# Performance work log

Measured on AMD Instinct MI355X. Metric: run time of the kernel, lower is better.

## Reference

```python
import jax, jax.numpy as jnp
import numpy as np
from itertools import product

# Static geometry (matches init_kwargs)
Z, H, W = 8, 96, 180
WZ, WH, WW = 2, 6, 12
MZ, MH, MW = Z // WZ, H // WH, W // WW   # 4, 16, 15
WP = WZ * WH * WW                        # 144 tokens per window
WN = MZ * MH * MW                        # 960 windows
DIM, HEADS = 384, 12
DH = DIM // HEADS
SHIFT = (WZ // 2, WH // 2, WW // 2)      # (1, 3, 6)
NBIAS = WZ * WZ * WH * WH * (2 * WW - 1) # 3312 bias entries
WT = MZ * MH                             # 64 window types (vary with Z,H only)


def _position_index():
    zi = np.arange(WZ); zj = -np.arange(WZ) * WZ
    hi = np.arange(WH); hj = -np.arange(WH) * WH
    w = np.arange(WW)
    c1 = np.stack(np.meshgrid(zi, hi, w, indexing='ij')).reshape(3, WP, 1)
    c2 = np.stack(np.meshgrid(zj, hj, w, indexing='ij')).reshape(3, 1, WP)
    coords = (c1 - c2).transpose(1, 2, 0).astype(np.int64)  # (WP, WP, 3)
    coords[:, :, 2] += WW - 1
    coords[:, :, 1] *= 2 * WW - 1
    coords[:, :, 0] *= (2 * WW - 1) * WH * WH
    return coords.sum(-1).reshape(-1)  # (WP*WP,)


def _attention_mask():
    # in_shape divisible by window -> pad mask is all-zero; only shifted-window
    # (non-adjacency) mask remains, exactly as in the torch buffer.
    img = np.ones((Z, H, W), np.float32)
    zs = (slice(0, -WZ), slice(-WZ, -SHIFT[0]), slice(-SHIFT[0], None))
    hs = (slice(0, -WH), slice(-WH, -SHIFT[1]), slice(-SHIFT[1], None))
    ws = (slice(0, -WW), slice(-WW, -SHIFT[2]), slice(-SHIFT[2], None))
    cnt = 0
    for z, h, w in product(zs, hs, ws):
        img[z, h, w] = cnt
        cnt += 1
    mw = img.reshape(MZ, WZ, MH, WH, MW, WW).transpose(0, 2, 4, 1, 3, 5).reshape(WN, WP)
    diff = mw[:, None, :] - mw[:, :, None]
    return np.where(diff != 0, -100.0, 0.0).astype(np.float32)


POS_IDX = jnp.asarray(_position_index())
ATTN_MASK = jnp.asarray(_attention_mask())  # (WN, WP, WP)


def _layernorm(x, w, b, eps=1e-5):
    m = jnp.mean(x, axis=-1, keepdims=True)
    v = jnp.mean(jnp.square(x - m), axis=-1, keepdims=True)
    return (x - m) * jax.lax.rsqrt(v + eps) * w + b


def setup_inputs() -> dict:
    key = jax.random.key(0)
    ks = jax.random.split(key, 8)
    s = 0.02
    return {
        'x': jax.random.normal(ks[0], (1, Z * H * W, DIM), jnp.float32),
        'w_qkv': jax.random.normal(ks[1], (DIM, 3 * DIM), jnp.float32) * s,
        'w_proj': jax.random.normal(ks[2], (DIM, DIM), jnp.float32) * s,
        'b_proj': jnp.zeros((DIM,), jnp.float32),
        'bias_table': jax.random.normal(ks[3], (NBIAS, WT, HEADS), jnp.float32) * 0.02,
        'ln1_w': jnp.ones((DIM,), jnp.float32),
        'ln1_b': jnp.zeros((DIM,), jnp.float32),
        'ln2_w': jnp.ones((DIM,), jnp.float32),
        'ln2_b': jnp.zeros((DIM,), jnp.float32),
        'w1': jax.random.normal(ks[4], (DIM, 4 * DIM), jnp.float32) * s,
        'b1': jnp.zeros((4 * DIM,), jnp.float32),
        'w2': jax.random.normal(ks[5], (4 * DIM, DIM), jnp.float32) * s,
        'b2': jnp.zeros((DIM,), jnp.float32),
    }


def reference(x, w_qkv, w_proj, b_proj, bias_table, ln1_w, ln1_b, ln2_w, ln2_b, w1, b1, w2, b2):
    B = x.shape[0]
    shortcut = x
    # (B, Z*H*W, D) -> (B, Z, H, W, D); pad is identity (divisible shapes)
    xg = x.reshape(B, Z, H, W, DIM)
    xg = jnp.roll(xg, (-SHIFT[0], -SHIFT[1], -SHIFT[2]), axis=(1, 2, 3))
    # window partition -> (B*WN, WP, D) with window order (B, mZ, mH, mW)
    xw = xg.reshape(B, MZ, WZ, MH, WH, MW, WW, DIM)
    xw = xw.transpose(0, 1, 3, 5, 2, 4, 6, 7).reshape(B * WN, WP, DIM)

    # ---- EarthAttention3D ----
    qkv = (xw @ w_qkv).reshape(B * WN, WP, 3, HEADS, DH).transpose(2, 0, 3, 1, 4)
    q = qkv[0] * (DH ** -0.5)
    k, v = qkv[1], qkv[2]
    attn = jnp.einsum('bhid,bhjd->bhij', q, k)  # (B*WN, HEADS, WP, WP)

    # earth-specific bias: one bias per (mZ, mH) window type, shared over B, mW
    bias = bias_table[POS_IDX].reshape(WP, WP, WT, HEADS).transpose(2, 3, 0, 1)
    bias = bias.reshape(MZ, MH, HEADS, WP, WP)
    attn = attn.reshape(B, MZ, MH, MW, HEADS, WP, WP) + bias[None, :, :, None]

    # shifted-window mask
    attn = attn.reshape(B, WN, HEADS, WP, WP) + ATTN_MASK[None, :, None]
    attn = jax.nn.softmax(attn, axis=-1).reshape(B * WN, HEADS, WP, WP)

    out = jnp.einsum('bhij,bhjd->bhid', attn, v)
    out = out.transpose(0, 2, 1, 3).reshape(B * WN, WP, DIM)
    out = out @ w_proj + b_proj

    # ---- window reverse, unroll, crop (identity) ----
    xg = out.reshape(B, MZ, MH, MW, WZ, WH, WW, DIM)
    xg = xg.transpose(0, 1, 4, 2, 5, 3, 6, 7).reshape(B, Z, H, W, DIM)
    xg = jnp.roll(xg, SHIFT, axis=(1, 2, 3))
    attn_out = xg.reshape(B, Z * H * W, DIM)

    # Pangu post-norm residuals (drop_path prob = 0 -> identity)
    x = shortcut + _layernorm(attn_out, ln1_w, ln1_b)
    h = jax.nn.gelu(x @ w1 + b1, approximate=False) @ w2 + b2
    x = x + _layernorm(h, ln2_w, ln2_b)
    return x
```

## Files before the change

kernel.cpp:

```cpp
#include <hip/hip_runtime.h>
#include <hip/hip_bf16.h>
#include <math.h>

typedef __hip_bfloat16 bf16;
typedef __attribute__((ext_vector_type(4))) float f32x4;
typedef __attribute__((ext_vector_type(8))) short s16x8;
typedef __attribute__((ext_vector_type(4))) short s16x4;

#define DEVI __device__ __forceinline__

constexpr int ZD = 8, HD = 96, WD = 180;
constexpr int WZ = 2, WH = 6, WWn = 12;
constexpr int MZ = 4, MH = 16, MW = 15;
constexpr int WP = 144, WN = 960;
constexpr int DIM = 384, HEADS = 12, DH = 32;
constexpr int TOK = ZD * HD * WD;
constexpr size_t TOKDIM = (size_t)TOK * DIM;
constexpr int NC = 3, CM = TOK / NC;

DEVI short f2b(float f) {
    bf16 h = __float2bfloat16(f);
    return *reinterpret_cast<short*>(&h);
}

DEVI int row_to_token(int r) {
    int wn = r / WP;
    int p  = r - wn * WP;
    int mz = wn / (MH * MW);
    int rem = wn - mz * (MH * MW);
    int mh = rem / MW;
    int mw = rem - mh * MW;
    int lz = p / (WH * WWn);
    int rp = p - lz * (WH * WWn);
    int lh = rp / WWn;
    int lw = rp - lh * WWn;
    int zp = mz * WZ + lz + 1;  if (zp >= ZD) zp -= ZD;
    int hp = mh * WH + lh + 3;  if (hp >= HD) hp -= HD;
    int wp = mw * WWn + lw + 6; if (wp >= WD) wp -= WD;
    return (zp * HD + hp) * WD + wp;
}


__global__ __launch_bounds__(256)
void k_fill(float* __restrict__ out, int n, float v) {
    int i = blockIdx.x * blockDim.x + threadIdx.x;
    if (i < n) out[i] = v;
}

__global__ __launch_bounds__(256)
void k_wcast(const float* __restrict__ w, bf16* __restrict__ wt, int K, int N) {
    int idx = blockIdx.x * blockDim.x + threadIdx.x;
    if (idx >= K * N) return;
    int n = idx / K;
    int k = idx - n * K;
    wt[idx] = __float2bfloat16(w[(size_t)k * N + n]);
}

__global__ __launch_bounds__(256)
void k_btr(const float* __restrict__ bt, float* __restrict__ btr) {
    int idx = blockIdx.x * blockDim.x + threadIdx.x;
    if (idx >= 64 * 12 * 3312) return;
    int wth = idx / 3312;
    int pos = idx - wth * 3312;
    btr[idx] = bt[(size_t)pos * 768 + wth] * 1.4426950408889634f;
}

__global__ __launch_bounds__(256)
void k_mktab(const float* __restrict__ btr, bf16* __restrict__ tab) {
    int idx = blockIdx.x * blockDim.x + threadIdx.x;
    if (idx >= 768 * WP * WP) return;
    int t = idx / (WP * WP);
    int e = idx - t * (WP * WP);
    int i = e / WP, j = e - i * WP;
    int wt = t / 12;
    int mz = wt >> 4, mh = wt & 15;
    int lzi = i / 72, ri_ = i - lzi * 72, lhi = ri_ / 12, lwi = ri_ - lhi * 12;
    int lzj = j / 72, rj_ = j - lzj * 72, lhj = rj_ / 12, lwj = rj_ - lhj * 12;
    int cA = lzi * 828 + lhi * 23 + lwi;
    int cB = lzj * 1656 + lhj * 138 + (11 - lwj);
    float vv = btr[(size_t)t * 3312 + cA + cB];
    int zri = (mz == 3) ? (lzi + 1) : 0, zrj = (mz == 3) ? (lzj + 1) : 0;
    int hri = (mh == 15) ? (lhi < 3 ? 1 : 2) : 0, hrj = (mh == 15) ? (lhj < 3 ? 1 : 2) : 0;
    if (zri != zrj || hri != hrj) vv -= 144.26950408889634f;
    tab[idx] = __float2bfloat16(vv);
}

__global__ __launch_bounds__(256)
void k_gather_x(const float* __restrict__ x, bf16* __restrict__ xw) {
    int idx = blockIdx.x * blockDim.x + threadIdx.x;
    if (idx >= TOK * 96) return;
    int r  = idx / 96;
    int c4 = (idx - r * 96) * 4;
    int t  = row_to_token(r);
    const float4 vv = *(const float4*)(x + (size_t)t * DIM + c4);
    s16x4 o;
    o[0] = f2b(vv.x); o[1] = f2b(vv.y); o[2] = f2b(vv.z); o[3] = f2b(vv.w);
    *(s16x4*)((short*)xw + (size_t)r * DIM + c4) = o;
}


DEVI void gload16(const bf16* g, bf16* l) {
    __builtin_amdgcn_global_load_lds(
        (const __attribute__((address_space(1))) void*)g,
        (__attribute__((address_space(3))) void*)l, 16, 0, 0);
}

template <int EPI>
__global__ __launch_bounds__(256)
void k_gemm(const bf16* __restrict__ A, const bf16* __restrict__ BT,
            const float* __restrict__ bias, bf16* __restrict__ out,
            int M, int N, int K) {
    constexpr int BK = 64;
    __shared__ bf16 As[128 * BK];
    __shared__ bf16 Bs[128 * BK];

    const int nb = N >> 7;
    const int g = blockIdx.x;
    const int xcd = g & 7;
    const int ii = g >> 3;
    const int tt = ii / nb;
    const int bm = tt * 8 + xcd;
    const int bn = ii - tt * nb;

    const int tid = threadIdx.x;
    const int lane = tid & 63;
    const int wv = tid >> 6;
    const int wr = wv >> 1, wc = wv & 1;
    const int lg = lane >> 4, lc = lane & 15;

    const bf16* Ab = A + (size_t)bm * 128 * K;
    const bf16* Bb = BT + (size_t)bn * 128 * K;

    f32x4 acc[4][4];
#pragma unroll
    for (int mi = 0; mi < 4; mi++)
#pragma unroll
        for (int ni = 0; ni < 4; ni++) acc[mi][ni] = {0.f, 0.f, 0.f, 0.f};

    const int kiters = K / BK;
    const int srow = (lane >> 3);
    const int scol = (lane & 7) * 8;

    for (int kt = 0; kt < kiters; kt++) {
        const int k0 = kt * BK;
#pragma unroll
        for (int i = 0; i < 4; i++) {
            int ch = wv * 4 + i;
            int row = ch * 8 + srow;
            gload16(Ab + (size_t)row * K + k0 + scol, &As[ch * 512]);
            gload16(Bb + (size_t)row * K + k0 + scol, &Bs[ch * 512]);
        }
        asm volatile("s_waitcnt vmcnt(0)" ::: "memory");
        __syncthreads();
#pragma unroll
        for (int kk = 0; kk < 2; kk++) {
            s16x8 af[4], bfv[4];
#pragma unroll
            for (int mi = 0; mi < 4; mi++)
                af[mi] = *(const s16x8*)&As[(64 * wr + 16 * mi + lc) * BK + kk * 32 + 8 * lg];
#pragma unroll
            for (int ni = 0; ni < 4; ni++)
                bfv[ni] = *(const s16x8*)&Bs[(64 * wc + 16 * ni + lc) * BK + kk * 32 + 8 * lg];
#pragma unroll
            for (int mi = 0; mi < 4; mi++)
#pragma unroll
                for (int ni = 0; ni < 4; ni++)
                    acc[mi][ni] = __builtin_amdgcn_mfma_f32_16x16x32_bf16(
                        af[mi], bfv[ni], acc[mi][ni], 0, 0, 0);
        }
        __syncthreads();
    }

    const int rbase = bm * 128 + 64 * wr + 4 * lg;
    const int cbase = bn * 128 + 64 * wc + lc;
#pragma unroll
    for (int mi = 0; mi < 4; mi++) {
#pragma unroll
        for (int ni = 0; ni < 4; ni++) {
            const int gc = cbase + 16 * ni;
#pragma unroll
            for (int r2 = 0; r2 < 4; r2++) {
                const int gr = rbase + 16 * mi + r2;
                float val = acc[mi][ni][r2];
                if constexpr (EPI == 0) {
                    int which = gc / DIM;
                    int remc = gc - which * DIM;
                    int hh = remc >> 5, dh = remc & 31;
                    if (which == 0) val *= 0.25503527f;
                    int wn = gr / WP;
                    int p = gr - wn * WP;
                    out[(size_t)which * TOKDIM +
                        ((size_t)(wn * HEADS + hh) * WP + p) * DH + dh] = __float2bfloat16(val);
                } else if constexpr (EPI == 1) {
                    val += bias[gc];
                    out[(size_t)gr * N + gc] = __float2bfloat16(val);
                } else {
                    val += bias[gc];
                    val = 0.5f * val * (1.0f + erff(val * 0.70710678118654752f));
                    out[(size_t)gr * N + gc] = __float2bfloat16(val);
                }
            }
        }
    }
}

__global__ __launch_bounds__(192)
void k_attn(const bf16* __restrict__ q, const bf16* __restrict__ kmat,
            const bf16* __restrict__ v, const bf16* __restrict__ tab,
            bf16* __restrict__ out) {
    __shared__ bf16 Ks[WP * DH];
    __shared__ bf16 VTs[DH * 168];
    __shared__ bf16 Ps[3][16][168];
    __shared__ unsigned char regn[WP];

    const int bid = blockIdx.x;
    const int wn = bid / HEADS, head = bid - wn * HEADS;
    const int mz = wn / (MH * MW);
    const int rem = wn - mz * (MH * MW);
    const int mh = rem / MW, mw = rem - (rem / MW) * MW;
    const int tile = (mz * MH + mh) * HEADS + head;

    const int tid = threadIdx.x;
    const int lane = tid & 63;
    const int s = tid >> 6;
    const int lg = lane >> 4, lc = lane & 15;

    const size_t base = (size_t)(wn * HEADS + head) * (WP * DH);
    {
        short* vt = (short*)VTs;
#pragma unroll
        for (int e2 = 0; e2 < 3; e2++) {
            int idx = tid + 192 * e2;
            *(s16x8*)(Ks + idx * 8) = *(const s16x8*)(kmat + base + idx * 8);
            s16x8 vv = *(const s16x8*)(v + base + idx * 8);
            int p = idx >> 2;
            int d0 = (idx & 3) * 8;
#pragma unroll
            for (int e = 0; e < 8; e++) vt[(d0 + e) * 168 + p] = vv[e];
        }
        { int d = tid / 6, rm = tid - d * 6;
          *(s16x4*)(vt + d * 168 + 144 + rm * 4) = (s16x4){0, 0, 0, 0}; }
        { short* pz = (short*)&Ps[s][0][0];
          *(s16x4*)(pz + (lane >> 2) * 168 + 144 + (lane & 3) * 4) = (s16x4){0, 0, 0, 0}; }
        if (tid < WP) {
            int lz = tid / 72, rp = tid - lz * 72;
            int lh = rp / 12, lw = rp - lh * 12;
            int zr = (mz == 3) ? (lz + 1) : 0;
            int hr = (mh == 15) ? (lh < 3 ? 1 : 2) : 0;
            int wbit = (lw < 6) ? 1 : 2;
            regn[tid] = (unsigned char)((zr * 3 + hr) * 4 + wbit);
        }
    }
    __syncthreads();

    const f32x4 zf = {0.f, 0.f, 0.f, 0.f};
    const bf16* tb = tab + (size_t)tile * (WP * WP);
    bf16* ob = out + (size_t)wn * (WP * DIM) + head * DH;
    short* ps = (short*)&Ps[s][0][0];
    const bf16* psb = &Ps[s][0][0];

    for (int t = 0; t < 3; t++) {
        const int strip = 3 * s + t;
        const int ib = 16 * strip + 4 * lg;
        s16x8 aq = *(const s16x8*)(q + base + (size_t)(16 * strip + lc) * DH + 8 * lg);
        f32x4 sacc[9];
#pragma unroll
        for (int jt = 0; jt < 9; jt++) {
            s16x8 bk = *(const s16x8*)(Ks + (16 * jt + lc) * DH + 8 * lg);
            sacc[jt] = __builtin_amdgcn_mfma_f32_16x16x32_bf16(aq, bk, zf, 0, 0, 0);
        }
#pragma unroll
        for (int jt = 0; jt < 9; jt++) {
            int j = 16 * jt + lc;
#pragma unroll
            for (int r2 = 0; r2 < 4; r2++)
                sacc[jt][r2] += __bfloat162float(tb[(ib + r2) * WP + j]);
        }
        if (mw == 14) {
            int ri[4];
#pragma unroll
            for (int r2 = 0; r2 < 4; r2++) ri[r2] = regn[ib + r2];
#pragma unroll
            for (int jt = 0; jt < 9; jt++) {
                int rj = regn[16 * jt + lc];
#pragma unroll
                for (int r2 = 0; r2 < 4; r2++) {
                    bool m = ((ri[r2] >> 2) == (rj >> 2)) && ((ri[r2] & 3) != (rj & 3));
                    if (m) sacc[jt][r2] -= 144.2695f;
                }
            }
        }
        float inv[4];
#pragma unroll
        for (int r2 = 0; r2 < 4; r2++) {
            float sum = 0.f;
#pragma unroll
            for (int jt = 0; jt < 9; jt++) {
                float pe = exp2f(sacc[jt][r2]);
                sacc[jt][r2] = pe;
                sum += pe;
            }
#pragma unroll
            for (int o = 1; o < 16; o <<= 1) sum += __shfl_xor(sum, o);
            inv[r2] = 1.0f / sum;
        }
#pragma unroll
        for (int jt = 0; jt < 9; jt++)
#pragma unroll
            for (int r2 = 0; r2 < 4; r2++)
                ps[(4 * lg + r2) * 168 + 16 * jt + lc] = f2b(sacc[jt][r2]);
        f32x4 oacc[2] = {zf, zf};
#pragma unroll
        for (int c = 0; c < 5; c++) {
            s16x8 ap = *(const s16x8*)(psb + lc * 168 + 32 * c + 8 * lg);
#pragma unroll
            for (int nt = 0; nt < 2; nt++) {
                s16x8 bv = *(const s16x8*)(VTs + (16 * nt + lc) * 168 + 32 * c + 8 * lg);
                oacc[nt] = __builtin_amdgcn_mfma_f32_16x16x32_bf16(ap, bv, oacc[nt], 0, 0, 0);
            }
        }
#pragma unroll
        for (int nt = 0; nt < 2; nt++)
#pragma unroll
            for (int r2 = 0; r2 < 4; r2++)
                ob[(size_t)(ib + r2) * DIM + 16 * nt + lc] =
                    __float2bfloat16(oacc[nt][r2] * inv[r2]);
    }
}


__global__ __launch_bounds__(128)
void k_ln1(const bf16* __restrict__ y, const float* __restrict__ x,
           const float* __restrict__ w, const float* __restrict__ b,
           bf16* __restrict__ x1b, int r0) {
    __shared__ float red[4];
    const int rl = blockIdx.x, tid = threadIdx.x;
    const int t = row_to_token(r0 + rl);
    float v[3];
#pragma unroll
    for (int e = 0; e < 3; e++) v[e] = __bfloat162float(y[(size_t)rl * DIM + tid + 128 * e]);
    float s = v[0] + v[1] + v[2];
    float s2 = v[0] * v[0] + v[1] * v[1] + v[2] * v[2];
#pragma unroll
    for (int o = 1; o < 64; o <<= 1) { s += __shfl_xor(s, o); s2 += __shfl_xor(s2, o); }
    const int wv = tid >> 6;
    if ((tid & 63) == 0) { red[wv * 2] = s; red[wv * 2 + 1] = s2; }
    __syncthreads();
    s = red[0] + red[2]; s2 = red[1] + red[3];
    float mean = s * (1.f / 384.f);
    float var = fmaxf(s2 * (1.f / 384.f) - mean * mean, 0.f);
    float rs = rsqrtf(var + 1e-5f);
#pragma unroll
    for (int e = 0; e < 3; e++) {
        int c = tid + 128 * e;
        float o = (v[e] - mean) * rs * w[c] + b[c];
        float xo = x[(size_t)t * DIM + c] + o;
        ((short*)x1b)[(size_t)t * DIM + c] = f2b(xo);
    }
}

__global__ __launch_bounds__(128)
void k_ln2(const bf16* __restrict__ h, const bf16* __restrict__ x1b,
           const float* __restrict__ w, const float* __restrict__ b,
           float* __restrict__ out) {
    __shared__ float red[4];
    const int r = blockIdx.x, tid = threadIdx.x;
    float v[3];
#pragma unroll
    for (int e = 0; e < 3; e++) v[e] = __bfloat162float(h[(size_t)r * DIM + tid + 128 * e]);
    float s = v[0] + v[1] + v[2];
    float s2 = v[0] * v[0] + v[1] * v[1] + v[2] * v[2];
#pragma unroll
    for (int o = 1; o < 64; o <<= 1) { s += __shfl_xor(s, o); s2 += __shfl_xor(s2, o); }
    const int wv = tid >> 6;
    if ((tid & 63) == 0) { red[wv * 2] = s; red[wv * 2 + 1] = s2; }
    __syncthreads();
    s = red[0] + red[2]; s2 = red[1] + red[3];
    float mean = s * (1.f / 384.f);
    float var = fmaxf(s2 * (1.f / 384.f) - mean * mean, 0.f);
    float rs = rsqrtf(var + 1e-5f);
#pragma unroll
    for (int e = 0; e < 3; e++) {
        int c = tid + 128 * e;
        float o = (v[e] - mean) * rs * w[c] + b[c];
        out[(size_t)r * DIM + c] = __bfloat162float(x1b[(size_t)r * DIM + c]) + o;
    }
}


extern "C" void kernel_launch(void* const* d_in, const int* in_sizes, int n_in,
                              void* d_out, int out_size, void* d_ws, size_t ws_size,
                              hipStream_t stream) {
    const float* x      = (const float*)d_in[0];
    const float* w_qkv  = (const float*)d_in[1];
    const float* w_proj = (const float*)d_in[2];
    const float* b_proj = (const float*)d_in[3];
    const float* btab   = (const float*)d_in[4];
    const float* ln1w   = (const float*)d_in[5];
    const float* ln1b   = (const float*)d_in[6];
    const float* ln2w   = (const float*)d_in[7];
    const float* ln2b   = (const float*)d_in[8];
    const float* w1     = (const float*)d_in[9];
    const float* b1     = (const float*)d_in[10];
    const float* w2     = (const float*)d_in[11];
    const float* b2     = (const float*)d_in[12];

    const size_t NEED = 470237184ULL;
    if (ws_size < NEED) {
        k_fill<<<(out_size + 255) / 256, 256, 0, stream>>>((float*)d_out, out_size, 12345.0f);
        return;
    }

    char* ws = (char*)d_ws;
    bf16* wqkvT  = (bf16*)(ws + 0);
    bf16* wprojT = (bf16*)(ws + 884736);
    bf16* w1T    = (bf16*)(ws + 1179648);
    bf16* w2T    = (bf16*)(ws + 2359296);
    float* btr   = (float*)(ws + 3538944);
    bf16* tab    = (bf16*)(ws + 13713408);

    const size_t D1 = 45563904;
    const size_t D2 = 364068864;

    bf16* qkv  = (bf16*)(ws + D1);
    bf16* x1b  = (bf16*)(ws + D1);
    bf16* ytmp = (bf16*)(ws + D1 + 106168320);
    bf16* h1c  = (bf16*)(ws + D1 + 106168320);
    bf16* xw   = (bf16*)(ws + D2);
    bf16* aout = (bf16*)(ws + D2);
    bf16* htmp = (bf16*)(ws + D2);

    k_wcast<<<(442368 + 255) / 256, 256, 0, stream>>>(w_qkv, wqkvT, 384, 1152);
    k_wcast<<<(147456 + 255) / 256, 256, 0, stream>>>(w_proj, wprojT, 384, 384);
    k_wcast<<<(589824 + 255) / 256, 256, 0, stream>>>(w1, w1T, 384, 1536);
    k_wcast<<<(589824 + 255) / 256, 256, 0, stream>>>(w2, w2T, 1536, 384);
    k_btr<<<(2543616 + 255) / 256, 256, 0, stream>>>(btab, btr);
    k_mktab<<<(768 * WP * WP + 255) / 256, 256, 0, stream>>>(btr, tab);
    k_gather_x<<<(TOK * 96 + 255) / 256, 256, 0, stream>>>(x, xw);

    k_gemm<0><<<dim3((TOK / 128) * 9), 256, 0, stream>>>(xw, wqkvT, nullptr, qkv, TOK, 1152, 384);

    k_attn<<<dim3(WN * HEADS), 192, 0, stream>>>(qkv, qkv + TOKDIM, qkv + 2 * TOKDIM, tab, aout);

    for (int c = 0; c < NC; c++) {
        k_gemm<1><<<dim3((CM / 128) * 3), 256, 0, stream>>>(
            aout + (size_t)c * CM * DIM, wprojT, b_proj, ytmp, CM, 384, 384);
        k_ln1<<<dim3(CM), 128, 0, stream>>>(ytmp, x, ln1w, ln1b, x1b, c * CM);
    }

    for (int c = 0; c < NC; c++) {
        k_gemm<2><<<dim3((CM / 128) * 12), 256, 0, stream>>>(
            x1b + (size_t)c * CM * DIM, w1T, b1, h1c, CM, 1536, 384);
        k_gemm<1><<<dim3((CM / 128) * 3), 256, 0, stream>>>(
            h1c, w2T, b2, htmp + (size_t)c * CM * DIM, CM, 384, 1536);
    }

    k_ln2<<<dim3(TOK), 128, 0, stream>>>(htmp, x1b, ln2w, ln2b, (float*)d_out);
}
```

Baseline: 1.441 ms.

## Switch GEMM to 32x32x16 MFMA with swizzled LDS and vectorized epilogue stores

The main GEMM kernel now uses 32x32x16 bf16 MFMA tiles in place of 16x16x32, with 2x2 accumulators per wave. Operands are swapped so the output lanes map to tokens and the accumulator rows map to features. LDS columns are XOR-swizzled to cut bank conflicts, and the epilogues write 4 contiguous bf16 values per store with vector bias loads. The intent is fewer MFMA and LDS instructions, fewer bank conflicts and wider global stores. The cost is a more complex index mapping, and the swizzle must match the unchanged load pattern exactly.

```diff
diff --git a/kernel.cpp b/kernel.cpp
--- a/kernel.cpp
+++ b/kernel.cpp
@@ -4,6 +4,7 @@
 
 typedef __hip_bfloat16 bf16;
 typedef __attribute__((ext_vector_type(4))) float f32x4;
+typedef __attribute__((ext_vector_type(16))) float f32x16;
 typedef __attribute__((ext_vector_type(8))) short s16x8;
 typedef __attribute__((ext_vector_type(4))) short s16x4;
 
@@ -125,21 +126,25 @@
     const int tid = threadIdx.x;
     const int lane = tid & 63;
     const int wv = tid >> 6;
-    const int wr = wv >> 1, wc = wv & 1;
-    const int lg = lane >> 4, lc = lane & 15;
+    const int wr = wv >> 1;
+    const int wc = wv & 1;
+    const int l31 = lane & 31, hi = lane >> 5;
 
     const bf16* Ab = A + (size_t)bm * 128 * K;
     const bf16* Bb = BT + (size_t)bn * 128 * K;
 
-    f32x4 acc[4][4];
-#pragma unroll
-    for (int mi = 0; mi < 4; mi++)
-#pragma unroll
-        for (int ni = 0; ni < 4; ni++) acc[mi][ni] = {0.f, 0.f, 0.f, 0.f};
+    f32x16 acc[2][2] = {{{}, {}}, {{}, {}}};
 
     const int kiters = K / BK;
-    const int srow = (lane >> 3);
-    const int scol = (lane & 7) * 8;
+    const int srow = lane >> 3;
+    const int scol = ((lane & 7) ^ srow) * 8;
+
+    int ra[2], rb[2], rax[2], rbx[2];
+#pragma unroll
+    for (int i2 = 0; i2 < 2; i2++) {
+        ra[i2] = 64 * wr + 32 * i2 + l31; rax[i2] = ra[i2] & 7;
+        rb[i2] = 64 * wc + 32 * i2 + l31; rbx[i2] = rb[i2] & 7;
+    }
 
     for (int kt = 0; kt < kiters; kt++) {
         const int k0 = kt * BK;
@@ -153,51 +158,66 @@
         asm volatile("s_waitcnt vmcnt(0)" ::: "memory");
         __syncthreads();
 #pragma unroll
-        for (int kk = 0; kk < 2; kk++) {
-            s16x8 af[4], bfv[4];
-#pragma unroll
-            for (int mi = 0; mi < 4; mi++)
-                af[mi] = *(const s16x8*)&As[(64 * wr + 16 * mi + lc) * BK + kk * 32 + 8 * lg];
-#pragma unroll
-            for (int ni = 0; ni < 4; ni++)
-                bfv[ni] = *(const s16x8*)&Bs[(64 * wc + 16 * ni + lc) * BK + kk * 32 + 8 * lg];
-#pragma unroll
-            for (int mi = 0; mi < 4; mi++)
-#pragma unroll
-                for (int ni = 0; ni < 4; ni++)
-                    acc[mi][ni] = __builtin_amdgcn_mfma_f32_16x16x32_bf16(
-                        af[mi], bfv[ni], acc[mi][ni], 0, 0, 0);
+        for (int kk = 0; kk < 4; kk++) {
+            const int s0 = 2 * kk + hi;
+            s16x8 af[2], bfv[2];
+#pragma unroll
+            for (int ni = 0; ni < 2; ni++)
+                af[ni] = *(const s16x8*)&Bs[ra[ni] * BK + ((s0 ^ rax[ni]) * 8)];
+#pragma unroll
+            for (int mi = 0; mi < 2; mi++)
+                bfv[mi] = *(const s16x8*)&As[rb[mi] * BK + ((s0 ^ rbx[mi]) * 8)];
+#pragma unroll
+            for (int ni = 0; ni < 2; ni++)
+#pragma unroll
+                for (int mi = 0; mi < 2; mi++)
+                    acc[ni][mi] = __builtin_amdgcn_mfma_f32_32x32x16_bf16(
+                        af[ni], bfv[mi], acc[ni][mi], 0, 0, 0);
         }
         __syncthreads();
     }
 
-    const int rbase = bm * 128 + 64 * wr + 4 * lg;
-    const int cbase = bn * 128 + 64 * wc + lc;
-#pragma unroll
-    for (int mi = 0; mi < 4; mi++) {
-#pragma unroll
-        for (int ni = 0; ni < 4; ni++) {
-            const int gc = cbase + 16 * ni;
-#pragma unroll
-            for (int r2 = 0; r2 < 4; r2++) {
-                const int gr = rbase + 16 * mi + r2;
-                float val = acc[mi][ni][r2];
+    const int tokbase = bm * 128 + 64 * wc + l31;
+    const int featbase = bn * 128 + 64 * wr + 4 * hi;
+#pragma unroll
+    for (int ni = 0; ni < 2; ni++) {
+#pragma unroll
+        for (int mi = 0; mi < 2; mi++) {
+            const int tok = tokbase + 32 * mi;
+#pragma unroll
+            for (int rq = 0; rq < 4; rq++) {
+                const int f0 = featbase + 32 * ni + 8 * rq;
+                float v0 = acc[ni][mi][4 * rq + 0];
+                float v1 = acc[ni][mi][4 * rq + 1];
+                float v2 = acc[ni][mi][4 * rq + 2];
+                float v3 = acc[ni][mi][4 * rq + 3];
                 if constexpr (EPI == 0) {
-                    int which = gc / DIM;
-                    int remc = gc - which * DIM;
-                    int hh = remc >> 5, dh = remc & 31;
-                    if (which == 0) val *= 0.25503527f;
-                    int wn = gr / WP;
-                    int p = gr - wn * WP;
-                    out[(size_t)which * TOKDIM +
-                        ((size_t)(wn * HEADS + hh) * WP + p) * DH + dh] = __float2bfloat16(val);
+                    const int which = f0 / DIM;
+                    const int rem = f0 - which * DIM;
+                    const int head = rem >> 5, dh = rem & 31;
+                    if (which == 0) {
+                        v0 *= 0.25503527f; v1 *= 0.25503527f;
+                        v2 *= 0.25503527f; v3 *= 0.25503527f;
+                    }
+                    const int wn = tok / WP, p = tok - wn * WP;
+                    s16x4 o; o[0] = f2b(v0); o[1] = f2b(v1); o[2] = f2b(v2); o[3] = f2b(v3);
+                    *(s16x4*)(out + (size_t)which * TOKDIM +
+                              ((size_t)(wn * HEADS + head) * WP + p) * DH + dh) = o;
                 } else if constexpr (EPI == 1) {
-                    val += bias[gc];
-                    out[(size_t)gr * N + gc] = __float2bfloat16(val);
+                    const float4 bv = *(const float4*)(bias + f0);
+                    s16x4 o;
+                    o[0] = f2b(v0 + bv.x); o[1] = f2b(v1 + bv.y);
+                    o[2] = f2b(v2 + bv.z); o[3] = f2b(v3 + bv.w);
+                    *(s16x4*)(out + (size_t)tok * N + f0) = o;
                 } else {
-                    val += bias[gc];
-                    val = 0.5f * val * (1.0f + erff(val * 0.70710678118654752f));
-                    out[(size_t)gr * N + gc] = __float2bfloat16(val);
+                    const float4 bv = *(const float4*)(bias + f0);
+                    float g0 = v0 + bv.x, g1 = v1 + bv.y, g2 = v2 + bv.z, g3 = v3 + bv.w;
+                    g0 = 0.5f * g0 * (1.0f + erff(g0 * 0.70710678118654752f));
+                    g1 = 0.5f * g1 * (1.0f + erff(g1 * 0.70710678118654752f));
+                    g2 = 0.5f * g2 * (1.0f + erff(g2 * 0.70710678118654752f));
+                    g3 = 0.5f * g3 * (1.0f + erff(g3 * 0.70710678118654752f));
+                    s16x4 o; o[0] = f2b(g0); o[1] = f2b(g1); o[2] = f2b(g2); o[3] = f2b(g3);
+                    *(s16x4*)(out + (size_t)tok * N + f0) = o;
                 }
             }
         }
```

Result: no change. 1.428 ms (-0.9%).
